# Optimization experiments

Hardware: AMD Instinct MI355X
Metric: run time of the kernel (lower is better)

The kernel has to match this reference:

```python
import jax, jax.numpy as jnp
import numpy as np

E = 8          # num_experts
TOP_K = 2
H = 2048       # hidden_size
F = 4096       # intermediate_size
T = 8192       # tokens (batch*seq flattened)


def setup_inputs() -> dict:
    key = jax.random.key(0)
    ks = jax.random.split(key, 5)
    s_h = 1.0 / np.sqrt(H)
    s_f = 1.0 / np.sqrt(F)
    return {
        "hidden_states": jax.random.normal(ks[0], (T, H), jnp.float32),
        "gate_w": jax.random.normal(ks[1], (E, H), jnp.float32) * s_h,   # Linear weight [out=E, in=H]
        "w1": jax.random.normal(ks[2], (E, F, H), jnp.float32) * s_h,    # per-expert [out=F, in=H]
        "w3": jax.random.normal(ks[3], (E, F, H), jnp.float32) * s_h,
        "w2": jax.random.normal(ks[4], (E, H, F), jnp.float32) * s_f,    # per-expert [out=H, in=F]
    }


def reference(hidden_states, gate_w, w1, w3, w2):
    x = hidden_states  # [T, H]
    router_logits = x @ gate_w.T                                  # [T, E]
    probs = jax.nn.softmax(router_logits, axis=-1)
    topk_w, topk_ids = jax.lax.top_k(probs, TOP_K)                # [T, K]
    topk_w = topk_w / jnp.sum(topk_w, axis=-1, keepdims=True)     # renormalize (top_k > 1)
    out = jnp.zeros_like(x)
    for e in range(E):  # small fixed expert loop, matches naive masked-dense MoE
        w_e = jnp.sum(topk_w * (topk_ids == e), axis=-1, keepdims=True)  # [T, 1]
        h = jax.nn.silu(x @ w1[e].T) * (x @ w3[e].T)              # [T, F] SwiGLU
        out = out + (h @ w2[e].T) * w_e                           # [T, H]
    return out
```

## Files before the change

### kernel.cpp

```cpp
#include <hip/hip_runtime.h>

#define T_TOK 8192
#define H_DIM 2048
#define F_DIM 4096
#define NE 8
#define NSLOT (T_TOK * 2)
#define BK 64

using bf16x8 = __attribute__((ext_vector_type(8))) __bf16;
using f32x4  = __attribute__((ext_vector_type(4))) float;
using u16x4  = __attribute__((ext_vector_type(4))) unsigned short;

__device__ __forceinline__ unsigned short f2bf(float f) {
  unsigned int u = __float_as_uint(f);
  unsigned int r = (u + 0x7FFFu + ((u >> 16) & 1u)) >> 16;
  return (unsigned short)r;
}

__device__ __forceinline__ void gload_lds16(const void* g, void* l) {
  __builtin_amdgcn_global_load_lds(
      (const __attribute__((address_space(1))) void*)g,
      (__attribute__((address_space(3))) void*)l, 16, 0, 0);
}

__global__ void k_zero(int* counts) {
  if (threadIdx.x < NE) counts[threadIdx.x] = 0;
}

__global__ void k_cast_x(const float* __restrict__ x, unsigned short* __restrict__ xbf) {
  const int n4 = T_TOK * H_DIM / 4;
  for (int i = blockIdx.x * 256 + threadIdx.x; i < n4; i += gridDim.x * 256) {
    f32x4 v = ((const f32x4*)x)[i];
    u16x4 o;
    o[0] = f2bf(v[0]); o[1] = f2bf(v[1]); o[2] = f2bf(v[2]); o[3] = f2bf(v[3]);
    ((u16x4*)xbf)[i] = o;
  }
}

__global__ __launch_bounds__(256) void k_router(
    const float* __restrict__ x, const float* __restrict__ gw,
    int* __restrict__ counts, int* __restrict__ eids, float* __restrict__ wts) {
  const int wave = threadIdx.x >> 6, lane = threadIdx.x & 63;
  const int tok = blockIdx.x * 4 + wave;
  const float* xr = x + (size_t)tok * H_DIM;
  float acc[NE];
  #pragma unroll
  for (int e = 0; e < NE; ++e) acc[e] = 0.f;
  for (int j = 0; j < H_DIM / 64; ++j) {
    int i = j * 64 + lane;
    float xv = xr[i];
    #pragma unroll
    for (int e = 0; e < NE; ++e) acc[e] += xv * gw[e * H_DIM + i];
  }
  #pragma unroll
  for (int e = 0; e < NE; ++e) {
    float v = acc[e];
    #pragma unroll
    for (int o = 32; o >= 1; o >>= 1) v += __shfl_xor(v, o);
    acc[e] = v;
  }
  int e0 = 0; float l0 = acc[0];
  #pragma unroll
  for (int e = 1; e < NE; ++e) if (acc[e] > l0) { l0 = acc[e]; e0 = e; }
  int e1 = -1; float l1 = -3.4e38f;
  #pragma unroll
  for (int e = 0; e < NE; ++e) if (e != e0 && acc[e] > l1) { l1 = acc[e]; e1 = e; }
  if (lane == 0) {
    float w0 = 1.f / (1.f + expf(l1 - l0));
    eids[2 * tok] = e0; eids[2 * tok + 1] = e1;
    wts[2 * tok] = w0;  wts[2 * tok + 1] = 1.f - w0;
    atomicAdd(&counts[e0], 1); atomicAdd(&counts[e1], 1);
  }
}

__global__ void k_prefix(const int* __restrict__ counts, int* __restrict__ offsets,
                         int* __restrict__ cursors) {
  if (threadIdx.x == 0) {
    int s = 0;
    for (int e = 0; e < NE; ++e) { offsets[e] = s; cursors[e] = s; s += counts[e]; }
    offsets[NE] = s;
  }
}

__global__ void k_scatter(const int* __restrict__ eids, const float* __restrict__ wts,
                          int* __restrict__ cursors, int* __restrict__ token_list,
                          float* __restrict__ slot_w, int* __restrict__ slot_of) {
  int t = blockIdx.x * 256 + threadIdx.x;
  if (t >= T_TOK) return;
  #pragma unroll
  for (int k = 0; k < 2; ++k) {
    int e = eids[2 * t + k];
    int pos = atomicAdd(&cursors[e], 1);
    token_list[pos] = t;
    slot_w[pos] = wts[2 * t + k];
    slot_of[2 * t + k] = pos;
  }
}

__global__ __launch_bounds__(256) void k_gemm1(
    const unsigned short* __restrict__ xbf,
    const float* __restrict__ w1, const float* __restrict__ w3,
    const int* __restrict__ offsets, const int* __restrict__ token_list,
    unsigned short* __restrict__ hbuf)
{
  const int e   = blockIdx.z;
  const int off = offsets[e];
  const int n_e = offsets[e + 1] - off;
  const int m0  = blockIdx.y * 128;
  if (m0 >= n_e) return;
  const int n0  = blockIdx.x * 128;

  __shared__ alignas(16) char lds[16384 + 32768];
  char* ldsA = lds;
  char* ldsB = lds + 16384;

  const int t = threadIdx.x, lane = t & 63, wave = t >> 6;

  const unsigned short* aSrc[4];
  #pragma unroll
  for (int j = 0; j < 4; ++j) {
    int row = j * 32 + (t >> 3);
    int sl  = (t & 7) ^ (row & 7);
    int mg  = m0 + row;
    int tok = (mg < n_e) ? token_list[off + mg] : 0;
    aSrc[j] = xbf + (size_t)tok * H_DIM + sl * 8;
  }
  const int c    = t & 15;
  const int nsub = t >> 4;
  const int bbase = nsub * 128 + (((c >> 1) ^ (nsub & 7)) << 4) + (c & 1) * 8;
  const int wboff = (n0 + nsub) * H_DIM + c * 4;
  const float* w1e = w1 + (size_t)e * F_DIM * H_DIM;
  const float* w3e = w3 + (size_t)e * F_DIM * H_DIM;

  const int lo = lane & 15, hi = lane >> 4;
  const int wm = (wave >> 1) * 64, wn = (wave & 1) * 64;
  const int rbaseA = (wm + lo) * 128;
  const int rbaseB = (wn + lo) * 128;
  const int x0 = ((hi    ) ^ (lo & 7)) << 4;
  const int x1 = ((hi + 4) ^ (lo & 7)) << 4;

  f32x4 accg[4][4], accu[4][4];
  const f32x4 zero = {0.f, 0.f, 0.f, 0.f};
  #pragma unroll
  for (int m = 0; m < 4; ++m)
    #pragma unroll
    for (int n = 0; n < 4; ++n) { accg[m][n] = zero; accu[m][n] = zero; }

  for (int k0 = 0; k0 < H_DIM; k0 += BK) {
    #pragma unroll
    for (int j = 0; j < 4; ++j)
      gload_lds16(aSrc[j] + k0, ldsA + j * 4096 + wave * 1024);
    #pragma unroll
    for (int i = 0; i < 8; ++i) {
      f32x4 v = *(const f32x4*)(w1e + wboff + i * (16 * H_DIM) + k0);
      u16x4 o;
      o[0] = f2bf(v[0]); o[1] = f2bf(v[1]); o[2] = f2bf(v[2]); o[3] = f2bf(v[3]);
      *(u16x4*)(ldsB + i * 2048 + bbase) = o;
    }
    #pragma unroll
    for (int i = 0; i < 8; ++i) {
      f32x4 v = *(const f32x4*)(w3e + wboff + i * (16 * H_DIM) + k0);
      u16x4 o;
      o[0] = f2bf(v[0]); o[1] = f2bf(v[1]); o[2] = f2bf(v[2]); o[3] = f2bf(v[3]);
      *(u16x4*)(ldsB + 16384 + i * 2048 + bbase) = o;
    }
    __syncthreads();
    #pragma unroll
    for (int kk = 0; kk < 2; ++kk) {
      const int xk = kk ? x1 : x0;
      bf16x8 af[4];
      #pragma unroll
      for (int m = 0; m < 4; ++m)
        af[m] = *(const bf16x8*)(ldsA + rbaseA + m * 2048 + xk);
      #pragma unroll
      for (int n = 0; n < 4; ++n) {
        bf16x8 b1 = *(const bf16x8*)(ldsB +         rbaseB + n * 2048 + xk);
        bf16x8 b3 = *(const bf16x8*)(ldsB + 16384 + rbaseB + n * 2048 + xk);
        #pragma unroll
        for (int m = 0; m < 4; ++m) {
          accg[m][n] = __builtin_amdgcn_mfma_f32_16x16x32_bf16(af[m], b1, accg[m][n], 0, 0, 0);
          accu[m][n] = __builtin_amdgcn_mfma_f32_16x16x32_bf16(af[m], b3, accu[m][n], 0, 0, 0);
        }
      }
    }
    __syncthreads();
  }
  #pragma unroll
  for (int m = 0; m < 4; ++m) {
    #pragma unroll
    for (int r = 0; r < 4; ++r) {
      int mg = m0 + wm + m * 16 + hi * 4 + r;
      if (mg < n_e) {
        unsigned short* dst = hbuf + (size_t)(off + mg) * F_DIM + n0 + wn + lo;
        #pragma unroll
        for (int n = 0; n < 4; ++n) {
          float g = accg[m][n][r];
          float u = accu[m][n][r];
          float h = (g / (1.f + expf(-g))) * u;
          dst[n * 16] = f2bf(h);
        }
      }
    }
  }
}

__global__ __launch_bounds__(256) void k_gemm2(
    const unsigned short* __restrict__ hbuf, const float* __restrict__ w2,
    const int* __restrict__ offsets, const float* __restrict__ slot_w,
    float* __restrict__ part)
{
  const int e   = blockIdx.z;
  const int off = offsets[e];
  const int n_e = offsets[e + 1] - off;
  const int m0  = blockIdx.y * 128;
  if (m0 >= n_e) return;
  const int n0  = blockIdx.x * 128;

  __shared__ alignas(16) char lds[32768];
  char* ldsA = lds;
  char* ldsB = lds + 16384;

  const int t = threadIdx.x, lane = t & 63, wave = t >> 6;

  const unsigned short* aSrc[4];
  #pragma unroll
  for (int j = 0; j < 4; ++j) {
    int row = j * 32 + (t >> 3);
    int sl  = (t & 7) ^ (row & 7);
    int mg  = m0 + row; if (mg >= n_e) mg = n_e - 1;
    aSrc[j] = hbuf + (size_t)(off + mg) * F_DIM + sl * 8;
  }
  const int c    = t & 15;
  const int nsub = t >> 4;
  const int bbase = nsub * 128 + (((c >> 1) ^ (nsub & 7)) << 4) + (c & 1) * 8;
  const int wboff = (n0 + nsub) * F_DIM + c * 4;
  const float* w2e = w2 + (size_t)e * H_DIM * F_DIM;

  const int lo = lane & 15, hi = lane >> 4;
  const int wm = (wave >> 1) * 64, wn = (wave & 1) * 64;
  const int rbaseA = (wm + lo) * 128;
  const int rbaseB = (wn + lo) * 128;
  const int x0 = ((hi    ) ^ (lo & 7)) << 4;
  const int x1 = ((hi + 4) ^ (lo & 7)) << 4;

  f32x4 acc[4][4];
  const f32x4 zero = {0.f, 0.f, 0.f, 0.f};
  #pragma unroll
  for (int m = 0; m < 4; ++m)
    #pragma unroll
    for (int n = 0; n < 4; ++n) acc[m][n] = zero;

  for (int k0 = 0; k0 < F_DIM; k0 += BK) {
    #pragma unroll
    for (int j = 0; j < 4; ++j)
      gload_lds16(aSrc[j] + k0, ldsA + j * 4096 + wave * 1024);
    #pragma unroll
    for (int i = 0; i < 8; ++i) {
      f32x4 v = *(const f32x4*)(w2e + wboff + i * (16 * F_DIM) + k0);
      u16x4 o;
      o[0] = f2bf(v[0]); o[1] = f2bf(v[1]); o[2] = f2bf(v[2]); o[3] = f2bf(v[3]);
      *(u16x4*)(ldsB + i * 2048 + bbase) = o;
    }
    __syncthreads();
    #pragma unroll
    for (int kk = 0; kk < 2; ++kk) {
      const int xk = kk ? x1 : x0;
      bf16x8 af[4], bfr[4];
      #pragma unroll
      for (int m = 0; m < 4; ++m) af[m]  = *(const bf16x8*)(ldsA + rbaseA + m * 2048 + xk);
      #pragma unroll
      for (int n = 0; n < 4; ++n) bfr[n] = *(const bf16x8*)(ldsB + rbaseB + n * 2048 + xk);
      #pragma unroll
      for (int m = 0; m < 4; ++m)
        #pragma unroll
        for (int n = 0; n < 4; ++n)
          acc[m][n] = __builtin_amdgcn_mfma_f32_16x16x32_bf16(af[m], bfr[n], acc[m][n], 0, 0, 0);
    }
    __syncthreads();
  }
  #pragma unroll
  for (int m = 0; m < 4; ++m) {
    #pragma unroll
    for (int r = 0; r < 4; ++r) {
      int mg = m0 + wm + m * 16 + hi * 4 + r;
      if (mg < n_e) {
        int slot = off + mg;
        float sw = slot_w[slot];
        float* dst = part + (size_t)slot * H_DIM + n0 + wn + lo;
        #pragma unroll
        for (int n = 0; n < 4; ++n) dst[n * 16] = acc[m][n][r] * sw;
      }
    }
  }
}

__global__ __launch_bounds__(256) void k_combine(
    const float* __restrict__ part, const int* __restrict__ slot_of,
    float* __restrict__ out) {
  int tok = blockIdx.x;
  int s0 = slot_of[2 * tok], s1 = slot_of[2 * tok + 1];
  const f32x4* p0 = (const f32x4*)(part + (size_t)s0 * H_DIM);
  const f32x4* p1 = (const f32x4*)(part + (size_t)s1 * H_DIM);
  f32x4* o = (f32x4*)(out + (size_t)tok * H_DIM);
  for (int i = threadIdx.x; i < H_DIM / 4; i += 256) o[i] = p0[i] + p1[i];
}

extern "C" void kernel_launch(void* const* d_in, const int* in_sizes, int n_in,
                              void* d_out, int out_size, void* d_ws, size_t ws_size,
                              hipStream_t stream) {
  (void)in_sizes; (void)n_in; (void)out_size; (void)ws_size;
  const float* x  = (const float*)d_in[0];
  const float* gw = (const float*)d_in[1];
  const float* w1 = (const float*)d_in[2];
  const float* w3 = (const float*)d_in[3];
  const float* w2 = (const float*)d_in[4];
  float* out = (float*)d_out;

  char* ws = (char*)d_ws;
  size_t p = 0;
  auto alloc = [&](size_t bytes) -> char* {
    char* r = ws + p;
    p = (p + bytes + 255) & ~(size_t)255;
    return r;
  };
  int*   counts     = (int*)alloc(NE * 4);
  int*   cursors    = (int*)alloc(NE * 4);
  int*   offsets    = (int*)alloc((NE + 1) * 4);
  int*   eids       = (int*)alloc((size_t)NSLOT * 4);
  float* wts        = (float*)alloc((size_t)NSLOT * 4);
  int*   token_list = (int*)alloc((size_t)NSLOT * 4);
  float* slot_w     = (float*)alloc((size_t)NSLOT * 4);
  int*   slot_of    = (int*)alloc((size_t)NSLOT * 4);
  unsigned short* xbf  = (unsigned short*)alloc((size_t)T_TOK * H_DIM * 2);
  unsigned short* hbuf = (unsigned short*)alloc((size_t)NSLOT * F_DIM * 2);
  float*          part = (float*)alloc((size_t)NSLOT * H_DIM * 4);

  k_zero<<<dim3(1), dim3(64), 0, stream>>>(counts);
  k_cast_x<<<dim3(4096), dim3(256), 0, stream>>>(x, xbf);
  k_router<<<dim3(T_TOK / 4), dim3(256), 0, stream>>>(x, gw, counts, eids, wts);
  k_prefix<<<dim3(1), dim3(1), 0, stream>>>(counts, offsets, cursors);
  k_scatter<<<dim3(T_TOK / 256), dim3(256), 0, stream>>>(eids, wts, cursors, token_list,
                                                         slot_w, slot_of);
  k_gemm1<<<dim3(F_DIM / 128, 64, NE), dim3(256), 0, stream>>>(xbf, w1, w3, offsets,
                                                               token_list, hbuf);
  k_gemm2<<<dim3(H_DIM / 128, 64, NE), dim3(256), 0, stream>>>(hbuf, w2, offsets,
                                                               slot_w, part);
  k_combine<<<dim3(T_TOK), dim3(256), 0, stream>>>(part, slot_of, out);
}
```

Baseline: 2.788 ms.

## Pre-cast expert weights to bf16 in staged batches and atomically combine outputs

Expert weights w1/w3/w2 are now converted to bf16 once per expert group by separate cast kernels into a staging buffer, instead of being read as fp32 and converted inside every GEMM tile. The GEMMs can then load B tiles straight into LDS with direct global-to-LDS loads, which cuts repeated fp32 weight reads and conversion work across the M tiles. The part buffer and the combine kernel are removed: gemm2 now atomically adds weighted results into a zeroed output. The cost is extra cast passes and launches, plus float atomics that make the summation order nondeterministic.

```diff
diff --git a/kernel.cpp b/kernel.cpp
--- a/kernel.cpp
+++ b/kernel.cpp
@@ -6,6 +6,8 @@
 #define NE 8
 #define NSLOT (T_TOK * 2)
 #define BK 64
+#define FH (F_DIM * H_DIM)
+#define EPERPH 4
 
 using bf16x8 = __attribute__((ext_vector_type(8))) __bf16;
 using f32x4  = __attribute__((ext_vector_type(4))) float;
@@ -27,13 +29,35 @@
   if (threadIdx.x < NE) counts[threadIdx.x] = 0;
 }
 
-__global__ void k_cast_x(const float* __restrict__ x, unsigned short* __restrict__ xbf) {
-  const int n4 = T_TOK * H_DIM / 4;
+__global__ __launch_bounds__(256) void k_zero_out(float* __restrict__ out, int n4) {
+  const f32x4 z = {0.f, 0.f, 0.f, 0.f};
+  for (int i = blockIdx.x * 256 + threadIdx.x; i < n4; i += gridDim.x * 256)
+    ((f32x4*)out)[i] = z;
+}
+
+__global__ __launch_bounds__(256) void k_cast(const float* __restrict__ src,
+                                              unsigned short* __restrict__ dst, int n4) {
   for (int i = blockIdx.x * 256 + threadIdx.x; i < n4; i += gridDim.x * 256) {
-    f32x4 v = ((const f32x4*)x)[i];
+    f32x4 v = ((const f32x4*)src)[i];
     u16x4 o;
     o[0] = f2bf(v[0]); o[1] = f2bf(v[1]); o[2] = f2bf(v[2]); o[3] = f2bf(v[3]);
-    ((u16x4*)xbf)[i] = o;
+    ((u16x4*)dst)[i] = o;
+  }
+}
+
+__global__ __launch_bounds__(256) void k_cast_w13(
+    const float* __restrict__ w1, const float* __restrict__ w3,
+    unsigned short* __restrict__ dst, int e_base) {
+  const int n4 = EPERPH * 2 * FH / 4;
+  for (int i = blockIdx.x * 256 + threadIdx.x; i < n4; i += gridDim.x * 256) {
+    int el   = i >> 22;
+    int mat  = (i >> 21) & 1;
+    int off4 = i & 0x1FFFFF;
+    const float* src = (mat ? w3 : w1) + ((size_t)(e_base + el) << 23);
+    f32x4 v = ((const f32x4*)src)[off4];
+    u16x4 o;
+    o[0] = f2bf(v[0]); o[1] = f2bf(v[1]); o[2] = f2bf(v[2]); o[3] = f2bf(v[3]);
+    ((u16x4*)dst)[i] = o;
   }
 }
 
@@ -84,7 +108,7 @@
 
 __global__ void k_scatter(const int* __restrict__ eids, const float* __restrict__ wts,
                           int* __restrict__ cursors, int* __restrict__ token_list,
-                          float* __restrict__ slot_w, int* __restrict__ slot_of) {
+                          float* __restrict__ slot_w) {
   int t = blockIdx.x * 256 + threadIdx.x;
   if (t >= T_TOK) return;
   #pragma unroll
@@ -93,44 +117,45 @@
     int pos = atomicAdd(&cursors[e], 1);
     token_list[pos] = t;
     slot_w[pos] = wts[2 * t + k];
-    slot_of[2 * t + k] = pos;
   }
 }
 
 __global__ __launch_bounds__(256) void k_gemm1(
     const unsigned short* __restrict__ xbf,
-    const float* __restrict__ w1, const float* __restrict__ w3,
+    const unsigned short* __restrict__ wstage,
     const int* __restrict__ offsets, const int* __restrict__ token_list,
-    unsigned short* __restrict__ hbuf)
+    unsigned short* __restrict__ hbuf, int e_base)
 {
-  const int e   = blockIdx.z;
+  const int el  = blockIdx.z;
+  const int e   = e_base + el;
   const int off = offsets[e];
   const int n_e = offsets[e + 1] - off;
   const int m0  = blockIdx.y * 128;
   if (m0 >= n_e) return;
   const int n0  = blockIdx.x * 128;
 
-  __shared__ alignas(16) char lds[16384 + 32768];
-  char* ldsA = lds;
-  char* ldsB = lds + 16384;
+  __shared__ alignas(16) char lds[49152];
+  char* ldsA  = lds;
+  char* ldsB1 = lds + 16384;
+  char* ldsB3 = lds + 32768;
 
   const int t = threadIdx.x, lane = t & 63, wave = t >> 6;
 
   const unsigned short* aSrc[4];
+  const unsigned short* b1Src[4];
+  const unsigned short* b3Src[4];
+  const unsigned short* w1e = wstage + (size_t)el * 2 * FH;
+  const unsigned short* w3e = w1e + FH;
   #pragma unroll
   for (int j = 0; j < 4; ++j) {
     int row = j * 32 + (t >> 3);
     int sl  = (t & 7) ^ (row & 7);
     int mg  = m0 + row;
     int tok = (mg < n_e) ? token_list[off + mg] : 0;
-    aSrc[j] = xbf + (size_t)tok * H_DIM + sl * 8;
-  }
-  const int c    = t & 15;
-  const int nsub = t >> 4;
-  const int bbase = nsub * 128 + (((c >> 1) ^ (nsub & 7)) << 4) + (c & 1) * 8;
-  const int wboff = (n0 + nsub) * H_DIM + c * 4;
-  const float* w1e = w1 + (size_t)e * F_DIM * H_DIM;
-  const float* w3e = w3 + (size_t)e * F_DIM * H_DIM;
+    aSrc[j]  = xbf + (size_t)tok * H_DIM + sl * 8;
+    b1Src[j] = w1e + (size_t)(n0 + row) * H_DIM + sl * 8;
+    b3Src[j] = w3e + (size_t)(n0 + row) * H_DIM + sl * 8;
+  }
 
   const int lo = lane & 15, hi = lane >> 4;
   const int wm = (wave >> 1) * 64, wn = (wave & 1) * 64;
@@ -148,21 +173,10 @@
 
   for (int k0 = 0; k0 < H_DIM; k0 += BK) {
     #pragma unroll
-    for (int j = 0; j < 4; ++j)
-      gload_lds16(aSrc[j] + k0, ldsA + j * 4096 + wave * 1024);
-    #pragma unroll
-    for (int i = 0; i < 8; ++i) {
-      f32x4 v = *(const f32x4*)(w1e + wboff + i * (16 * H_DIM) + k0);
-      u16x4 o;
-      o[0] = f2bf(v[0]); o[1] = f2bf(v[1]); o[2] = f2bf(v[2]); o[3] = f2bf(v[3]);
-      *(u16x4*)(ldsB + i * 2048 + bbase) = o;
-    }
-    #pragma unroll
-    for (int i = 0; i < 8; ++i) {
-      f32x4 v = *(const f32x4*)(w3e + wboff + i * (16 * H_DIM) + k0);
-      u16x4 o;
-      o[0] = f2bf(v[0]); o[1] = f2bf(v[1]); o[2] = f2bf(v[2]); o[3] = f2bf(v[3]);
-      *(u16x4*)(ldsB + 16384 + i * 2048 + bbase) = o;
+    for (int j = 0; j < 4; ++j) {
+      gload_lds16(aSrc[j]  + k0, ldsA  + j * 4096 + wave * 1024);
+      gload_lds16(b1Src[j] + k0, ldsB1 + j * 4096 + wave * 1024);
+      gload_lds16(b3Src[j] + k0, ldsB3 + j * 4096 + wave * 1024);
     }
     __syncthreads();
     #pragma unroll
@@ -174,8 +188,8 @@
         af[m] = *(const bf16x8*)(ldsA + rbaseA + m * 2048 + xk);
       #pragma unroll
       for (int n = 0; n < 4; ++n) {
-        bf16x8 b1 = *(const bf16x8*)(ldsB +         rbaseB + n * 2048 + xk);
-        bf16x8 b3 = *(const bf16x8*)(ldsB + 16384 + rbaseB + n * 2048 + xk);
+        bf16x8 b1 = *(const bf16x8*)(ldsB1 + rbaseB + n * 2048 + xk);
+        bf16x8 b3 = *(const bf16x8*)(ldsB3 + rbaseB + n * 2048 + xk);
         #pragma unroll
         for (int m = 0; m < 4; ++m) {
           accg[m][n] = __builtin_amdgcn_mfma_f32_16x16x32_bf16(af[m], b1, accg[m][n], 0, 0, 0);
@@ -205,11 +219,12 @@
 }
 
 __global__ __launch_bounds__(256) void k_gemm2(
-    const unsigned short* __restrict__ hbuf, const float* __restrict__ w2,
-    const int* __restrict__ offsets, const float* __restrict__ slot_w,
-    float* __restrict__ part)
+    const unsigned short* __restrict__ hbuf, const unsigned short* __restrict__ wstage,
+    const int* __restrict__ offsets, const int* __restrict__ token_list,
+    const float* __restrict__ slot_w, float* __restrict__ out, int e_base)
 {
-  const int e   = blockIdx.z;
+  const int el  = blockIdx.z;
+  const int e   = e_base + el;
   const int off = offsets[e];
   const int n_e = offsets[e + 1] - off;
   const int m0  = blockIdx.y * 128;
@@ -223,18 +238,16 @@
   const int t = threadIdx.x, lane = t & 63, wave = t >> 6;
 
   const unsigned short* aSrc[4];
+  const unsigned short* bSrc[4];
+  const unsigned short* w2e = wstage + (size_t)el * FH;
   #pragma unroll
   for (int j = 0; j < 4; ++j) {
     int row = j * 32 + (t >> 3);
     int sl  = (t & 7) ^ (row & 7);
     int mg  = m0 + row; if (mg >= n_e) mg = n_e - 1;
     aSrc[j] = hbuf + (size_t)(off + mg) * F_DIM + sl * 8;
-  }
-  const int c    = t & 15;
-  const int nsub = t >> 4;
-  const int bbase = nsub * 128 + (((c >> 1) ^ (nsub & 7)) << 4) + (c & 1) * 8;
-  const int wboff = (n0 + nsub) * F_DIM + c * 4;
-  const float* w2e = w2 + (size_t)e * H_DIM * F_DIM;
+    bSrc[j] = w2e + (size_t)(n0 + row) * F_DIM + sl * 8;
+  }
 
   const int lo = lane & 15, hi = lane >> 4;
   const int wm = (wave >> 1) * 64, wn = (wave & 1) * 64;
@@ -252,14 +265,9 @@
 
   for (int k0 = 0; k0 < F_DIM; k0 += BK) {
     #pragma unroll
-    for (int j = 0; j < 4; ++j)
+    for (int j = 0; j < 4; ++j) {
       gload_lds16(aSrc[j] + k0, ldsA + j * 4096 + wave * 1024);
-    #pragma unroll
-    for (int i = 0; i < 8; ++i) {
-      f32x4 v = *(const f32x4*)(w2e + wboff + i * (16 * F_DIM) + k0);
-      u16x4 o;
-      o[0] = f2bf(v[0]); o[1] = f2bf(v[1]); o[2] = f2bf(v[2]); o[3] = f2bf(v[3]);
-      *(u16x4*)(ldsB + i * 2048 + bbase) = o;
+      gload_lds16(bSrc[j] + k0, ldsB + j * 4096 + wave * 1024);
     }
     __syncthreads();
     #pragma unroll
@@ -285,24 +293,15 @@
       int mg = m0 + wm + m * 16 + hi * 4 + r;
       if (mg < n_e) {
         int slot = off + mg;
+        int tok  = token_list[slot];
         float sw = slot_w[slot];
-        float* dst = part + (size_t)slot * H_DIM + n0 + wn + lo;
+        float* dst = out + (size_t)tok * H_DIM + n0 + wn + lo;
         #pragma unroll
-        for (int n = 0; n < 4; ++n) dst[n * 16] = acc[m][n][r] * sw;
+        for (int n = 0; n < 4; ++n)
+          unsafeAtomicAdd(&dst[n * 16], acc[m][n][r] * sw);
       }
     }
   }
-}
-
-__global__ __launch_bounds__(256) void k_combine(
-    const float* __restrict__ part, const int* __restrict__ slot_of,
-    float* __restrict__ out) {
-  int tok = blockIdx.x;
-  int s0 = slot_of[2 * tok], s1 = slot_of[2 * tok + 1];
-  const f32x4* p0 = (const f32x4*)(part + (size_t)s0 * H_DIM);
-  const f32x4* p1 = (const f32x4*)(part + (size_t)s1 * H_DIM);
-  f32x4* o = (f32x4*)(out + (size_t)tok * H_DIM);
-  for (int i = threadIdx.x; i < H_DIM / 4; i += 256) o[i] = p0[i] + p1[i];
 }
 
 extern "C" void kernel_launch(void* const* d_in, const int* in_sizes, int n_in,
@@ -330,20 +329,26 @@
   float* wts        = (float*)alloc((size_t)NSLOT * 4);
   int*   token_list = (int*)alloc((size_t)NSLOT * 4);
   float* slot_w     = (float*)alloc((size_t)NSLOT * 4);
-  int*   slot_of    = (int*)alloc((size_t)NSLOT * 4);
-  unsigned short* xbf  = (unsigned short*)alloc((size_t)T_TOK * H_DIM * 2);
-  unsigned short* hbuf = (unsigned short*)alloc((size_t)NSLOT * F_DIM * 2);
-  float*          part = (float*)alloc((size_t)NSLOT * H_DIM * 4);
+  unsigned short* xbf    = (unsigned short*)alloc((size_t)T_TOK * H_DIM * 2);
+  unsigned short* hbuf   = (unsigned short*)alloc((size_t)NSLOT * F_DIM * 2);
+  unsigned short* wstage = (unsigned short*)alloc((size_t)EPERPH * 2 * FH * 2);
 
   k_zero<<<dim3(1), dim3(64), 0, stream>>>(counts);
-  k_cast_x<<<dim3(4096), dim3(256), 0, stream>>>(x, xbf);
+  k_zero_out<<<dim3(2048), dim3(256), 0, stream>>>(out, T_TOK * H_DIM / 4);
+  k_cast<<<dim3(2048), dim3(256), 0, stream>>>(x, xbf, T_TOK * H_DIM / 4);
   k_router<<<dim3(T_TOK / 4), dim3(256), 0, stream>>>(x, gw, counts, eids, wts);
   k_prefix<<<dim3(1), dim3(1), 0, stream>>>(counts, offsets, cursors);
   k_scatter<<<dim3(T_TOK / 256), dim3(256), 0, stream>>>(eids, wts, cursors, token_list,
-                                                         slot_w, slot_of);
-  k_gemm1<<<dim3(F_DIM / 128, 64, NE), dim3(256), 0, stream>>>(xbf, w1, w3, offsets,
-                                                               token_list, hbuf);
-  k_gemm2<<<dim3(H_DIM / 128, 64, NE), dim3(256), 0, stream>>>(hbuf, w2, offsets,
-                                                               slot_w, part);
-  k_combine<<<dim3(T_TOK), dim3(256), 0, stream>>>(part, slot_of, out);
-}
+                                                         slot_w);
+  for (int eb = 0; eb < NE; eb += EPERPH) {
+    k_cast_w13<<<dim3(2048), dim3(256), 0, stream>>>(w1, w3, wstage, eb);
+    k_gemm1<<<dim3(F_DIM / 128, 64, EPERPH), dim3(256), 0, stream>>>(
+        xbf, wstage, offsets, token_list, hbuf, eb);
+  }
+  for (int eb = 0; eb < NE; eb += EPERPH) {
+    k_cast<<<dim3(2048), dim3(256), 0, stream>>>(
+        w2 + (size_t)eb * FH, wstage, EPERPH * FH / 4);
+    k_gemm2<<<dim3(H_DIM / 128, 64, EPERPH), dim3(256), 0, stream>>>(
+        hbuf, wstage, offsets, token_list, slot_w, out, eb);
+  }
+}
```

Result: no change. 2.742 ms (-1.6%).
